# Performance work log

Measured on AMD Instinct MI355X. Metric: run time of the kernel, lower is better.

The kernel has to match this reference:

```python
import jax, jax.numpy as jnp
import numpy as np

N = 100000      # number of vertices
E = 3200000     # number of directed edges (avg degree 32)
EPS = 1e-8
WEIGHT = 0.01


def setup_inputs() -> dict:
    key = jax.random.key(0)
    k1, k2, k3, k4 = jax.random.split(key, 4)
    mu0 = jax.random.normal(k1, (N, 3), dtype=jnp.float32)
    # current positions = canonical + small deformation (realistic ARAP setting)
    mu = mu0 + 0.1 * jax.random.normal(k2, (N, 3), dtype=jnp.float32)
    i = jax.random.randint(k3, (E,), 0, N, dtype=jnp.int32)
    # avoid self-edges (rest length 0 would give w = 1/eps = 1e8 and swamp the loss)
    off = jax.random.randint(k4, (E,), 1, N, dtype=jnp.int32)
    j = (i + off) % N
    edge_idx = jnp.stack([i, j], axis=0)  # (2, E)
    return {"mu0": mu0, "mu": mu, "edge_idx": edge_idx}


def reference(mu0, mu, edge_idx):
    i, j = edge_idx[0], edge_idx[1]
    rest = mu0[j] - mu0[i]        # (E,3) canonical edge vectors
    deform = mu[j] - mu[i]        # (E,3) deformed edge vectors
    w = 1.0 / (jnp.linalg.norm(rest, axis=-1) + EPS)  # (E,)
    # per-edge weighted outer product deform \otimes rest
    outer = jnp.einsum('e,ei,ej->eij', w, deform, rest)  # (E,3,3)
    # scatter-add into per-node covariance matrices
    S = jnp.zeros((mu0.shape[0], 3, 3), dtype=mu0.dtype).at[i].add(outer)  # (N,3,3)
    U, _, Vh = jnp.linalg.svd(S, full_matrices=False)
    R = U @ Vh
    det_mask = (jnp.linalg.det(R) < 0)[:, None, None]
    diag_fix = jnp.array([-1.0, 1.0, 1.0], dtype=mu0.dtype).reshape(1, 1, 3)
    Vh = jnp.where(det_mask, Vh * diag_fix, Vh)
    R = U @ Vh                      # (N,3,3) best-fit rotations
    Ri = R[i]                       # (E,3,3)
    pred = jnp.einsum('eij,ej->ei', Ri, rest)
    err = deform - pred
    loss = jnp.sum(w * jnp.sum(err * err, axis=-1)) / jnp.sum(w)
    return WEIGHT * loss
```

## Files before the change

kernel.cpp:

```cpp
#include <hip/hip_runtime.h>
#include <hip/hip_fp16.h>
#include <math.h>

#define EPS     1e-8f
#define MP      131
#define JBITS   17
#define JMASK   ((1u << JBITS) - 1u)
#define CAP     6144
#define PMAX    1024
#define ACC_T   576
#define MAXPT   11
#define BIN_T   512
#define CHUNK   8192
#define EPT     16

struct alignas(16) Pk { __half2 a, b, c; unsigned pad; };

__global__ __launch_bounds__(256) void k_prep(
    const float* __restrict__ mu0, const float* __restrict__ mu,
    Pk* __restrict__ pk, int* __restrict__ gcursor, int N, int P)
{
    int n = blockIdx.x * blockDim.x + threadIdx.x;
    if (n < P) gcursor[n] = n * CAP;
    if (n >= N) return;
    float x0 = mu0[3*n+0], y0 = mu0[3*n+1], z0 = mu0[3*n+2];
    float x1 = mu [3*n+0], y1 = mu [3*n+1], z1 = mu [3*n+2];
    Pk o;
    o.a = __floats2half2_rn(x0, y0);
    o.b = __floats2half2_rn(z0, x1);
    o.c = __floats2half2_rn(y1, z1);
    o.pad = 0u;
    pk[n] = o;
}

__global__ __launch_bounds__(BIN_T) void k_bin(
    const int* __restrict__ ei, const int* __restrict__ ej,
    int* __restrict__ gcursor, unsigned* __restrict__ bucket,
    int E, int P)
{
    __shared__ int cnt[PMAX];
    __shared__ int dbase[PMAX];
    __shared__ int scan_tmp[PMAX];
    __shared__ int wtot[8];
    __shared__ unsigned sortw[CHUNK];
    __shared__ unsigned short sortp[CHUNK];

    int lo = blockIdx.x * CHUNK;
    int hi = lo + CHUNK; if (hi > E) hi = E;
    int ce = hi - lo;
    int tid = threadIdx.x;

    for (int t = tid; t < PMAX; t += BIN_T) cnt[t] = 0;

    int myi[EPT], myj[EPT];
    #pragma unroll
    for (int k = 0; k < EPT; ++k) {
        int e = lo + tid + k * BIN_T;
        if (e < hi) {
            myi[k] = __builtin_nontemporal_load(&ei[e]);
            myj[k] = __builtin_nontemporal_load(&ej[e]);
        } else myi[k] = -1;
    }
    __syncthreads();

    #pragma unroll
    for (int k = 0; k < EPT; ++k)
        if (myi[k] >= 0) atomicAdd(&cnt[(unsigned)myi[k] / (unsigned)MP], 1);
    __syncthreads();

    {
        int b0 = 2 * tid;
        int v1 = cnt[b0 + 1];
        int s  = cnt[b0] + v1;
        int incl = s;
        #pragma unroll
        for (int d = 1; d < 64; d <<= 1) {
            int o = __shfl_up(incl, d);
            if ((tid & 63) >= d) incl += o;
        }
        int w = tid >> 6;
        if ((tid & 63) == 63) wtot[w] = incl;
        __syncthreads();
        int base = 0;
        #pragma unroll
        for (int k = 0; k < 8; ++k) base += (k < w) ? wtot[k] : 0;
        scan_tmp[b0]     = base + incl - v1;
        scan_tmp[b0 + 1] = base + incl;
        __syncthreads();
    }

    for (int t = tid; t < P; t += BIN_T) {
        int c = cnt[t];
        int excl = scan_tmp[t] - c;
        int b = c ? atomicAdd(&gcursor[t], c) : 0;
        dbase[t] = b - excl;
        cnt[t] = excl;
    }
    __syncthreads();

    #pragma unroll
    for (int k = 0; k < EPT; ++k) {
        if (myi[k] >= 0) {
            int i = myi[k];
            int p = (int)((unsigned)i / (unsigned)MP);
            int li = i - p * MP;
            int pos = atomicAdd(&cnt[p], 1);
            sortw[pos] = ((unsigned)li << JBITS) | (unsigned)myj[k];
            sortp[pos] = (unsigned short)p;
        }
    }
    __syncthreads();

    for (int s = tid; s < ce; s += BIN_T) {
        unsigned w = sortw[s];
        int p = sortp[s];
        int dst = dbase[p] + s;
        if (dst < (p + 1) * CAP)
            bucket[dst] = w;
    }
}

__global__ __launch_bounds__(ACC_T) void k_accum(
    const Pk* __restrict__ pk,
    const unsigned* __restrict__ bucket, const int* __restrict__ gcursor,
    double* __restrict__ pblk, int N)
{
    __shared__ unsigned sorted[CAP];
    __shared__ int hist[MP];
    __shared__ int offs[MP];
    __shared__ int cursor[MP];
    __shared__ int sc[192];
    __shared__ float Sl[MP * 9];
    __shared__ double redw[9], rede[9];

    int p = blockIdx.x;
    int lo_n = p * MP;
    int beg = p * CAP;
    int end = gcursor[p];
    int cap_end = beg + CAP;
    if (end > cap_end) end = cap_end;

    for (int t = threadIdx.x; t < MP; t += ACC_T) hist[t] = 0;
    __syncthreads();

    unsigned myu[MAXPT];
    int mycnt = 0;
    {
        int e = beg + threadIdx.x;
        #pragma unroll
        for (int k = 0; k < MAXPT; ++k) {
            if (e < end) {
                unsigned uu = bucket[e];
                myu[k] = uu;
                atomicAdd(&hist[uu >> JBITS], 1);
                ++mycnt;
            }
            e += ACC_T;
        }
    }
    __syncthreads();

    if (threadIdx.x < 192) {
        int v = (threadIdx.x < MP) ? hist[threadIdx.x] : 0;
        int incl = v;
        #pragma unroll
        for (int d = 1; d < 64; d <<= 1) {
            int o = __shfl_up(incl, d);
            if ((threadIdx.x & 63) >= d) incl += o;
        }
        sc[threadIdx.x] = incl;
    }
    __syncthreads();
    if (threadIdx.x < MP) {
        int w = threadIdx.x >> 6;
        int carry = 0;
        if (w >= 1) carry += sc[63];
        if (w >= 2) carry += sc[127];
        int excl = sc[threadIdx.x] - hist[threadIdx.x] + carry;
        offs[threadIdx.x] = excl;
        cursor[threadIdx.x] = excl;
    }
    __syncthreads();

    #pragma unroll
    for (int k = 0; k < MAXPT; ++k) {
        if (k < mycnt) {
            unsigned uu = myu[k];
            int li = (int)(uu >> JBITS);
            int pos = atomicAdd(&cursor[li], 1);
            sorted[pos] = uu;
        }
    }
    __syncthreads();

    double wsum = 0.0, errsum = 0.0;
    float S[9] = {0.f,0.f,0.f,0.f,0.f,0.f,0.f,0.f,0.f};
    {
        int node = threadIdx.x >> 2;
        int part = threadIdx.x & 3;
        int n = lo_n + node;
        if (node < MP && n < N) {
            Pk ac = pk[n];
            float2 a01 = __half22float2(ac.a);
            float2 a23 = __half22float2(ac.b);
            float2 a45 = __half22float2(ac.c);
            float ax = a01.x, ay = a01.y, az = a23.x;
            float cx = a23.y, cy = a45.x, cz = a45.y;

            auto body = [&](const Pk& cc) {
                float2 f01 = __half22float2(cc.a);
                float2 f23 = __half22float2(cc.b);
                float2 f45 = __half22float2(cc.c);
                float r0 = f01.x - ax, r1 = f01.y - ay, r2 = f23.x - az;
                float d0 = f23.y - cx, d1 = f45.x - cy, d2 = f45.y - cz;
                float rr = r0*r0 + r1*r1 + r2*r2;
                float dd = d0*d0 + d1*d1 + d2*d2;
                float w  = 1.0f / (sqrtf(rr) + EPS);
                wsum   += (double)w;
                errsum += (double)(w * (dd + rr));
                float wd0 = w*d0, wd1 = w*d1, wd2 = w*d2;
                S[0] += wd0*r0; S[1] += wd0*r1; S[2] += wd0*r2;
                S[3] += wd1*r0; S[4] += wd1*r1; S[5] += wd1*r2;
                S[6] += wd2*r0; S[7] += wd2*r1; S[8] += wd2*r2;
            };

            int b0 = offs[node];
            int e1 = b0 + hist[node];
            int e  = b0 + part;
            for (; e + 12 < e1; e += 16) {
                unsigned u0 = sorted[e];
                unsigned u1 = sorted[e + 4];
                unsigned u2 = sorted[e + 8];
                unsigned u3 = sorted[e + 12];
                Pk c0 = pk[u0 & JMASK];
                Pk c1 = pk[u1 & JMASK];
                Pk c2 = pk[u2 & JMASK];
                Pk c3 = pk[u3 & JMASK];
                body(c0); body(c1); body(c2); body(c3);
            }
            for (; e + 4 < e1; e += 8) {
                unsigned u0 = sorted[e], u1 = sorted[e + 4];
                Pk c0 = pk[u0 & JMASK];
                Pk c1 = pk[u1 & JMASK];
                body(c0);
                body(c1);
            }
            if (e < e1) {
                Pk c0 = pk[sorted[e] & JMASK];
                body(c0);
            }
        }
        #pragma unroll
        for (int c = 0; c < 9; ++c) {
            S[c] += __shfl_down(S[c], 2);
            S[c] += __shfl_down(S[c], 1);
        }
        if (part == 0 && node < MP)
            #pragma unroll
            for (int c = 0; c < 9; ++c) Sl[node*9 + c] = S[c];
    }
    __syncthreads();

    if (threadIdx.x < MP && lo_n + (int)threadIdx.x < N) {
        float Sf[9], X[9];
        #pragma unroll
        for (int c = 0; c < 9; ++c) { Sf[c] = Sl[threadIdx.x*9 + c]; X[c] = Sf[c]; }
        bool ok = true;
        #pragma unroll
        for (int it = 0; it < 8; ++it) {
            float c00 =  (X[4]*X[8] - X[5]*X[7]);
            float c01 = -(X[3]*X[8] - X[5]*X[6]);
            float c02 =  (X[3]*X[7] - X[4]*X[6]);
            float c10 = -(X[1]*X[8] - X[2]*X[7]);
            float c11 =  (X[0]*X[8] - X[2]*X[6]);
            float c12 = -(X[0]*X[7] - X[1]*X[6]);
            float c20 =  (X[1]*X[5] - X[2]*X[4]);
            float c21 = -(X[0]*X[5] - X[2]*X[3]);
            float c22 =  (X[0]*X[4] - X[1]*X[3]);
            float det = X[0]*c00 + X[1]*c01 + X[2]*c02;
            if (!(fabsf(det) > 1e-30f)) { ok = false; break; }
            float inv_det = 1.0f / det;
            float Y[9] = { c00*inv_det, c01*inv_det, c02*inv_det,
                           c10*inv_det, c11*inv_det, c12*inv_det,
                           c20*inv_det, c21*inv_det, c22*inv_det };
            float nx = 0.f, ny = 0.f;
            #pragma unroll
            for (int c = 0; c < 9; ++c) { nx += X[c]*X[c]; ny += Y[c]*Y[c]; }
            float g = sqrtf(sqrtf(ny / nx));
            float hg = 0.5f * g, hig = 0.5f / g;
            #pragma unroll
            for (int c = 0; c < 9; ++c) X[c] = hg * X[c] + hig * Y[c];
        }
        if (!ok) {
            X[0]=1.f; X[1]=0.f; X[2]=0.f;
            X[3]=0.f; X[4]=1.f; X[5]=0.f;
            X[6]=0.f; X[7]=0.f; X[8]=1.f;
        }
        float det = X[0]*(X[4]*X[8] - X[5]*X[7])
                  - X[1]*(X[3]*X[8] - X[5]*X[6])
                  + X[2]*(X[3]*X[7] - X[4]*X[6]);
        if (det < 0.f) { X[0] = -X[0]; X[3] = -X[3]; X[6] = -X[6]; }
        float tr = X[0]*Sf[0] + X[1]*Sf[1] + X[2]*Sf[2]
                 + X[3]*Sf[3] + X[4]*Sf[4] + X[5]*Sf[5]
                 + X[6]*Sf[6] + X[7]*Sf[7] + X[8]*Sf[8];
        errsum -= 2.0 * (double)tr;
    }

    #pragma unroll
    for (int off = 32; off > 0; off >>= 1) {
        wsum   += __shfl_down(wsum, off);
        errsum += __shfl_down(errsum, off);
    }
    if ((threadIdx.x & 63) == 0) {
        redw[threadIdx.x >> 6] = wsum;
        rede[threadIdx.x >> 6] = errsum;
    }
    __syncthreads();
    if (threadIdx.x == 0) {
        double W = 0.0, Er = 0.0;
        #pragma unroll
        for (int k = 0; k < 9; ++k) { W += redw[k]; Er += rede[k]; }
        pblk[2*p]   = W;
        pblk[2*p+1] = Er;
    }
}

__global__ __launch_bounds__(256) void k_final(
    const double* __restrict__ pblk, int nb, float* __restrict__ out)
{
    __shared__ double sw[4], se[4];
    double w = 0.0, e = 0.0;
    for (int t = threadIdx.x; t < nb; t += 256) {
        w += pblk[2*t];
        e += pblk[2*t+1];
    }
    #pragma unroll
    for (int off = 32; off > 0; off >>= 1) {
        w += __shfl_down(w, off);
        e += __shfl_down(e, off);
    }
    if ((threadIdx.x & 63) == 0) {
        sw[threadIdx.x >> 6] = w;
        se[threadIdx.x >> 6] = e;
    }
    __syncthreads();
    if (threadIdx.x == 0) {
        double W  = sw[0] + sw[1] + sw[2] + sw[3];
        double Er = se[0] + se[1] + se[2] + se[3];
        out[0] = (float)(0.01 * (Er / W));
    }
}

extern "C" void kernel_launch(void* const* d_in, const int* in_sizes, int n_in,
                              void* d_out, int out_size, void* d_ws, size_t ws_size,
                              hipStream_t stream) {
    const float* mu0 = (const float*)d_in[0];
    const float* mu  = (const float*)d_in[1];
    const int*   eidx = (const int*)d_in[2];
    int N = in_sizes[0] / 3;
    int E = in_sizes[2] / 2;
    const int* ei = eidx;
    const int* ej = eidx + E;

    int P = (N + MP - 1) / MP;

    double*   pblk    = (double*)d_ws;
    int*      gcursor = (int*)((char*)d_ws + 2 * PMAX * sizeof(double));
    Pk*       pk      = (Pk*)((char*)d_ws + 2 * PMAX * sizeof(double) + PMAX * sizeof(int));
    unsigned* bucket  = (unsigned*)(pk + N);

    int nbin = (E + CHUNK - 1) / CHUNK;

    k_prep  <<<(N + 255) / 256, 256, 0, stream>>>(mu0, mu, pk, gcursor, N, P);
    k_bin   <<<nbin, BIN_T, 0, stream>>>(ei, ej, gcursor, bucket, E, P);
    k_accum <<<P, ACC_T, 0, stream>>>(pk, bucket, gcursor, pblk, N);
    k_final <<<1, 256, 0, stream>>>(pblk, P, (float*)d_out);
}
```

Measured before the change: 139.7 us.

## Replace block-local binning with per-edge global atomics on padded cursors

The binning kernel no longer counts, scans and sorts edges in shared memory before a coalesced write. Each thread now takes one edge and claims a slot with a global atomicAdd on its partition cursor, and the cursors are padded to one per 64 bytes to avoid false sharing. The accumulate loop is also unrolled from 4 to 8 outstanding gathers. This removes the shared-memory scan and sort and their syncs, at the cost of about 3.2M global atomics on 764 hot addresses and scattered bucket writes.

```diff
diff --git a/kernel.cpp b/kernel.cpp
--- a/kernel.cpp
+++ b/kernel.cpp
@@ -8,11 +8,9 @@
 #define JMASK   ((1u << JBITS) - 1u)
 #define CAP     6144
 #define PMAX    1024
+#define GCS     16
 #define ACC_T   576
 #define MAXPT   11
-#define BIN_T   512
-#define CHUNK   8192
-#define EPT     16
 
 struct alignas(16) Pk { __half2 a, b, c; unsigned pad; };
 
@@ -21,7 +19,7 @@
     Pk* __restrict__ pk, int* __restrict__ gcursor, int N, int P)
 {
     int n = blockIdx.x * blockDim.x + threadIdx.x;
-    if (n < P) gcursor[n] = n * CAP;
+    if (n < P) gcursor[n * GCS] = n * CAP;
     if (n >= N) return;
     float x0 = mu0[3*n+0], y0 = mu0[3*n+1], z0 = mu0[3*n+2];
     float x1 = mu [3*n+0], y1 = mu [3*n+1], z1 = mu [3*n+2];
@@ -33,91 +31,19 @@
     pk[n] = o;
 }
 
-__global__ __launch_bounds__(BIN_T) void k_bin(
+__global__ __launch_bounds__(256) void k_bin(
     const int* __restrict__ ei, const int* __restrict__ ej,
-    int* __restrict__ gcursor, unsigned* __restrict__ bucket,
-    int E, int P)
+    int* __restrict__ gcursor, unsigned* __restrict__ bucket, int E)
 {
-    __shared__ int cnt[PMAX];
-    __shared__ int dbase[PMAX];
-    __shared__ int scan_tmp[PMAX];
-    __shared__ int wtot[8];
-    __shared__ unsigned sortw[CHUNK];
-    __shared__ unsigned short sortp[CHUNK];
-
-    int lo = blockIdx.x * CHUNK;
-    int hi = lo + CHUNK; if (hi > E) hi = E;
-    int ce = hi - lo;
-    int tid = threadIdx.x;
-
-    for (int t = tid; t < PMAX; t += BIN_T) cnt[t] = 0;
-
-    int myi[EPT], myj[EPT];
-    #pragma unroll
-    for (int k = 0; k < EPT; ++k) {
-        int e = lo + tid + k * BIN_T;
-        if (e < hi) {
-            myi[k] = __builtin_nontemporal_load(&ei[e]);
-            myj[k] = __builtin_nontemporal_load(&ej[e]);
-        } else myi[k] = -1;
-    }
-    __syncthreads();
-
-    #pragma unroll
-    for (int k = 0; k < EPT; ++k)
-        if (myi[k] >= 0) atomicAdd(&cnt[(unsigned)myi[k] / (unsigned)MP], 1);
-    __syncthreads();
-
-    {
-        int b0 = 2 * tid;
-        int v1 = cnt[b0 + 1];
-        int s  = cnt[b0] + v1;
-        int incl = s;
-        #pragma unroll
-        for (int d = 1; d < 64; d <<= 1) {
-            int o = __shfl_up(incl, d);
-            if ((tid & 63) >= d) incl += o;
-        }
-        int w = tid >> 6;
-        if ((tid & 63) == 63) wtot[w] = incl;
-        __syncthreads();
-        int base = 0;
-        #pragma unroll
-        for (int k = 0; k < 8; ++k) base += (k < w) ? wtot[k] : 0;
-        scan_tmp[b0]     = base + incl - v1;
-        scan_tmp[b0 + 1] = base + incl;
-        __syncthreads();
-    }
-
-    for (int t = tid; t < P; t += BIN_T) {
-        int c = cnt[t];
-        int excl = scan_tmp[t] - c;
-        int b = c ? atomicAdd(&gcursor[t], c) : 0;
-        dbase[t] = b - excl;
-        cnt[t] = excl;
-    }
-    __syncthreads();
-
-    #pragma unroll
-    for (int k = 0; k < EPT; ++k) {
-        if (myi[k] >= 0) {
-            int i = myi[k];
-            int p = (int)((unsigned)i / (unsigned)MP);
-            int li = i - p * MP;
-            int pos = atomicAdd(&cnt[p], 1);
-            sortw[pos] = ((unsigned)li << JBITS) | (unsigned)myj[k];
-            sortp[pos] = (unsigned short)p;
-        }
-    }
-    __syncthreads();
-
-    for (int s = tid; s < ce; s += BIN_T) {
-        unsigned w = sortw[s];
-        int p = sortp[s];
-        int dst = dbase[p] + s;
-        if (dst < (p + 1) * CAP)
-            bucket[dst] = w;
-    }
+    int e = blockIdx.x * 256 + threadIdx.x;
+    if (e >= E) return;
+    int i = __builtin_nontemporal_load(&ei[e]);
+    int j = __builtin_nontemporal_load(&ej[e]);
+    unsigned p = (unsigned)i / (unsigned)MP;
+    int li = i - (int)p * MP;
+    int pos = atomicAdd(&gcursor[p * GCS], 1);
+    if (pos < (int)(p + 1) * CAP)
+        bucket[pos] = ((unsigned)li << JBITS) | (unsigned)j;
 }
 
 __global__ __launch_bounds__(ACC_T) void k_accum(
@@ -136,7 +62,7 @@
     int p = blockIdx.x;
     int lo_n = p * MP;
     int beg = p * CAP;
-    int end = gcursor[p];
+    int end = gcursor[p * GCS];
     int cap_end = beg + CAP;
     if (end > cap_end) end = cap_end;
 
@@ -227,16 +153,25 @@
             int b0 = offs[node];
             int e1 = b0 + hist[node];
             int e  = b0 + part;
-            for (; e + 12 < e1; e += 16) {
+            for (; e + 28 < e1; e += 32) {
                 unsigned u0 = sorted[e];
                 unsigned u1 = sorted[e + 4];
                 unsigned u2 = sorted[e + 8];
                 unsigned u3 = sorted[e + 12];
+                unsigned u4 = sorted[e + 16];
+                unsigned u5 = sorted[e + 20];
+                unsigned u6 = sorted[e + 24];
+                unsigned u7 = sorted[e + 28];
                 Pk c0 = pk[u0 & JMASK];
                 Pk c1 = pk[u1 & JMASK];
                 Pk c2 = pk[u2 & JMASK];
                 Pk c3 = pk[u3 & JMASK];
+                Pk c4 = pk[u4 & JMASK];
+                Pk c5 = pk[u5 & JMASK];
+                Pk c6 = pk[u6 & JMASK];
+                Pk c7 = pk[u7 & JMASK];
                 body(c0); body(c1); body(c2); body(c3);
+                body(c4); body(c5); body(c6); body(c7);
             }
             for (; e + 4 < e1; e += 8) {
                 unsigned u0 = sorted[e], u1 = sorted[e + 4];
@@ -366,13 +301,12 @@
 
     double*   pblk    = (double*)d_ws;
     int*      gcursor = (int*)((char*)d_ws + 2 * PMAX * sizeof(double));
-    Pk*       pk      = (Pk*)((char*)d_ws + 2 * PMAX * sizeof(double) + PMAX * sizeof(int));
+    Pk*       pk      = (Pk*)((char*)d_ws + 2 * PMAX * sizeof(double)
+                                          + PMAX * GCS * sizeof(int));
     unsigned* bucket  = (unsigned*)(pk + N);
 
-    int nbin = (E + CHUNK - 1) / CHUNK;
-
     k_prep  <<<(N + 255) / 256, 256, 0, stream>>>(mu0, mu, pk, gcursor, N, P);
-    k_bin   <<<nbin, BIN_T, 0, stream>>>(ei, ej, gcursor, bucket, E, P);
+    k_bin   <<<(E + 255) / 256, 256, 0, stream>>>(ei, ej, gcursor, bucket, E);
     k_accum <<<P, ACC_T, 0, stream>>>(pk, bucket, gcursor, pblk, N);
     k_final <<<1, 256, 0, stream>>>(pblk, P, (float*)d_out);
 }
```

Result: slower. 291.9 us (+109.0%).

## Replace atomic global bucket cursors with deterministic histogram, column-scan and scatter passes

Applied to the files above, without the earlier changes.

Binning becomes three passes. A per-chunk histogram kernel also packs the node data, a per-partition column scan computes exact global offsets, and a scatter kernel writes edges to those offsets. This removes the global atomics on bucket cursors, makes the bucket layout contiguous and deterministic, and lets the per-partition capacity and registers-per-thread shrink. It also widens the accumulation unroll to 8 gathers and keeps per-thread weight and error sums in float instead of double, at the cost of an extra launch, a second read of the source index array, and some precision.

```diff
diff --git a/kernel.cpp b/kernel.cpp
--- a/kernel.cpp
+++ b/kernel.cpp
@@ -6,73 +6,122 @@
 #define MP      131
 #define JBITS   17
 #define JMASK   ((1u << JBITS) - 1u)
-#define CAP     6144
+#define CAP     5120
 #define PMAX    1024
+#define OTS     768
+#define NBMAX   512
 #define ACC_T   576
-#define MAXPT   11
+#define MAXPT   9
 #define BIN_T   512
 #define CHUNK   8192
 #define EPT     16
 
 struct alignas(16) Pk { __half2 a, b, c; unsigned pad; };
 
-__global__ __launch_bounds__(256) void k_prep(
+__global__ __launch_bounds__(BIN_T) void k_hist(
     const float* __restrict__ mu0, const float* __restrict__ mu,
-    Pk* __restrict__ pk, int* __restrict__ gcursor, int N, int P)
+    Pk* __restrict__ pk, const int* __restrict__ ei,
+    int* __restrict__ cntT, int E, int N, int P)
 {
-    int n = blockIdx.x * blockDim.x + threadIdx.x;
-    if (n < P) gcursor[n] = n * CAP;
-    if (n >= N) return;
-    float x0 = mu0[3*n+0], y0 = mu0[3*n+1], z0 = mu0[3*n+2];
-    float x1 = mu [3*n+0], y1 = mu [3*n+1], z1 = mu [3*n+2];
-    Pk o;
-    o.a = __floats2half2_rn(x0, y0);
-    o.b = __floats2half2_rn(z0, x1);
-    o.c = __floats2half2_rn(y1, z1);
-    o.pad = 0u;
-    pk[n] = o;
-}
-
-__global__ __launch_bounds__(BIN_T) void k_bin(
+    __shared__ int cnt[PMAX];
+    int tid = threadIdx.x;
+
+    for (int n = blockIdx.x * BIN_T + tid; n < N; n += gridDim.x * BIN_T) {
+        float x0 = mu0[3*n+0], y0 = mu0[3*n+1], z0 = mu0[3*n+2];
+        float x1 = mu [3*n+0], y1 = mu [3*n+1], z1 = mu [3*n+2];
+        Pk o;
+        o.a = __floats2half2_rn(x0, y0);
+        o.b = __floats2half2_rn(z0, x1);
+        o.c = __floats2half2_rn(y1, z1);
+        o.pad = 0u;
+        pk[n] = o;
+    }
+
+    for (int t = tid; t < PMAX; t += BIN_T) cnt[t] = 0;
+    __syncthreads();
+
+    int lo = blockIdx.x * CHUNK;
+    int hi = lo + CHUNK; if (hi > E) hi = E;
+    #pragma unroll
+    for (int k = 0; k < EPT; ++k) {
+        int e = lo + tid + k * BIN_T;
+        if (e < hi) {
+            int i = __builtin_nontemporal_load(&ei[e]);
+            atomicAdd(&cnt[(unsigned)i / (unsigned)MP], 1);
+        }
+    }
+    __syncthreads();
+
+    size_t bo = (size_t)blockIdx.x * OTS;
+    for (int t = tid; t < P; t += BIN_T) cntT[bo + t] = cnt[t];
+}
+
+__global__ __launch_bounds__(BIN_T) void k_colscan(
+    const int* __restrict__ cntT, int* __restrict__ gofs,
+    int* __restrict__ tend, int nbin)
+{
+    __shared__ int wtot[8];
+    int p = blockIdx.x;
+    int t = threadIdx.x;
+    int v = (t < nbin) ? cntT[(size_t)t * OTS + p] : 0;
+    int incl = v;
+    #pragma unroll
+    for (int d = 1; d < 64; d <<= 1) {
+        int o = __shfl_up(incl, d);
+        if ((t & 63) >= d) incl += o;
+    }
+    int w = t >> 6;
+    if ((t & 63) == 63) wtot[w] = incl;
+    __syncthreads();
+    int base = 0;
+    #pragma unroll
+    for (int k = 0; k < 8; ++k) base += (k < w) ? wtot[k] : 0;
+    int excl = base + incl - v;
+    if (t < nbin) gofs[(size_t)t * OTS + p] = p * CAP + excl;
+    if (t == nbin - 1) tend[p] = p * CAP + excl + v;
+}
+
+__global__ __launch_bounds__(BIN_T) void k_scatter(
     const int* __restrict__ ei, const int* __restrict__ ej,
-    int* __restrict__ gcursor, unsigned* __restrict__ bucket,
+    const int* __restrict__ gofs, unsigned* __restrict__ bucket,
     int E, int P)
 {
     __shared__ int cnt[PMAX];
     __shared__ int dbase[PMAX];
-    __shared__ int scan_tmp[PMAX];
     __shared__ int wtot[8];
     __shared__ unsigned sortw[CHUNK];
     __shared__ unsigned short sortp[CHUNK];
 
+    int tid = threadIdx.x;
     int lo = blockIdx.x * CHUNK;
     int hi = lo + CHUNK; if (hi > E) hi = E;
     int ce = hi - lo;
-    int tid = threadIdx.x;
 
     for (int t = tid; t < PMAX; t += BIN_T) cnt[t] = 0;
 
-    int myi[EPT], myj[EPT];
+    int myp[EPT]; unsigned myw[EPT];
     #pragma unroll
     for (int k = 0; k < EPT; ++k) {
         int e = lo + tid + k * BIN_T;
         if (e < hi) {
-            myi[k] = __builtin_nontemporal_load(&ei[e]);
-            myj[k] = __builtin_nontemporal_load(&ej[e]);
-        } else myi[k] = -1;
+            int i = __builtin_nontemporal_load(&ei[e]);
+            int j = __builtin_nontemporal_load(&ej[e]);
+            unsigned p = (unsigned)i / (unsigned)MP;
+            myp[k] = (int)p;
+            myw[k] = (((unsigned)i - p * MP) << JBITS) | (unsigned)j;
+        } else myp[k] = -1;
     }
     __syncthreads();
 
     #pragma unroll
     for (int k = 0; k < EPT; ++k)
-        if (myi[k] >= 0) atomicAdd(&cnt[(unsigned)myi[k] / (unsigned)MP], 1);
+        if (myp[k] >= 0) atomicAdd(&cnt[myp[k]], 1);
     __syncthreads();
 
     {
-        int b0 = 2 * tid;
-        int v1 = cnt[b0 + 1];
-        int s  = cnt[b0] + v1;
-        int incl = s;
+        int b0 = 2 * tid, b1 = b0 + 1;
+        int v0 = cnt[b0], v1 = cnt[b1];
+        int incl = v0 + v1;
         #pragma unroll
         for (int d = 1; d < 64; d <<= 1) {
             int o = __shfl_up(incl, d);
@@ -84,45 +133,42 @@
         int base = 0;
         #pragma unroll
         for (int k = 0; k < 8; ++k) base += (k < w) ? wtot[k] : 0;
-        scan_tmp[b0]     = base + incl - v1;
-        scan_tmp[b0 + 1] = base + incl;
-        __syncthreads();
-    }
-
-    for (int t = tid; t < P; t += BIN_T) {
-        int c = cnt[t];
-        int excl = scan_tmp[t] - c;
-        int b = c ? atomicAdd(&gcursor[t], c) : 0;
-        dbase[t] = b - excl;
-        cnt[t] = excl;
+        int inc1 = base + incl;
+        int inc0 = inc1 - v1;
+        cnt[b0] = inc0 - v0;
+        cnt[b1] = inc1 - v1;
+    }
+    __syncthreads();
+
+    {
+        size_t bo = (size_t)blockIdx.x * OTS;
+        for (int t = tid; t < P; t += BIN_T)
+            dbase[t] = gofs[bo + t] - cnt[t];
     }
     __syncthreads();
 
     #pragma unroll
     for (int k = 0; k < EPT; ++k) {
-        if (myi[k] >= 0) {
-            int i = myi[k];
-            int p = (int)((unsigned)i / (unsigned)MP);
-            int li = i - p * MP;
-            int pos = atomicAdd(&cnt[p], 1);
-            sortw[pos] = ((unsigned)li << JBITS) | (unsigned)myj[k];
-            sortp[pos] = (unsigned short)p;
+        if (myp[k] >= 0) {
+            int pos = atomicAdd(&cnt[myp[k]], 1);
+            sortw[pos] = myw[k];
+            sortp[pos] = (unsigned short)myp[k];
         }
     }
     __syncthreads();
 
     for (int s = tid; s < ce; s += BIN_T) {
-        unsigned w = sortw[s];
+        unsigned wv = sortw[s];
         int p = sortp[s];
         int dst = dbase[p] + s;
         if (dst < (p + 1) * CAP)
-            bucket[dst] = w;
+            bucket[dst] = wv;
     }
 }
 
 __global__ __launch_bounds__(ACC_T) void k_accum(
     const Pk* __restrict__ pk,
-    const unsigned* __restrict__ bucket, const int* __restrict__ gcursor,
+    const unsigned* __restrict__ bucket, const int* __restrict__ tend,
     double* __restrict__ pblk, int N)
 {
     __shared__ unsigned sorted[CAP];
@@ -136,7 +182,7 @@
     int p = blockIdx.x;
     int lo_n = p * MP;
     int beg = p * CAP;
-    int end = gcursor[p];
+    int end = tend[p];
     int cap_end = beg + CAP;
     if (end > cap_end) end = cap_end;
 
@@ -188,7 +234,7 @@
             unsigned uu = myu[k];
             int li = (int)(uu >> JBITS);
             int pos = atomicAdd(&cursor[li], 1);
-            sorted[pos] = uu;
+            if (pos < CAP) sorted[pos] = uu;
         }
     }
     __syncthreads();
@@ -199,6 +245,7 @@
         int node = threadIdx.x >> 2;
         int part = threadIdx.x & 3;
         int n = lo_n + node;
+        float ws = 0.f, es = 0.f;
         if (node < MP && n < N) {
             Pk ac = pk[n];
             float2 a01 = __half22float2(ac.a);
@@ -216,8 +263,8 @@
                 float rr = r0*r0 + r1*r1 + r2*r2;
                 float dd = d0*d0 + d1*d1 + d2*d2;
                 float w  = 1.0f / (sqrtf(rr) + EPS);
-                wsum   += (double)w;
-                errsum += (double)(w * (dd + rr));
+                ws += w;
+                es += w * (dd + rr);
                 float wd0 = w*d0, wd1 = w*d1, wd2 = w*d2;
                 S[0] += wd0*r0; S[1] += wd0*r1; S[2] += wd0*r2;
                 S[3] += wd1*r0; S[4] += wd1*r1; S[5] += wd1*r2;
@@ -226,17 +273,27 @@
 
             int b0 = offs[node];
             int e1 = b0 + hist[node];
+            if (e1 > CAP) e1 = CAP;
             int e  = b0 + part;
-            for (; e + 12 < e1; e += 16) {
+            for (; e + 28 < e1; e += 32) {
                 unsigned u0 = sorted[e];
                 unsigned u1 = sorted[e + 4];
                 unsigned u2 = sorted[e + 8];
                 unsigned u3 = sorted[e + 12];
+                unsigned u4 = sorted[e + 16];
+                unsigned u5 = sorted[e + 20];
+                unsigned u6 = sorted[e + 24];
+                unsigned u7 = sorted[e + 28];
                 Pk c0 = pk[u0 & JMASK];
                 Pk c1 = pk[u1 & JMASK];
                 Pk c2 = pk[u2 & JMASK];
                 Pk c3 = pk[u3 & JMASK];
+                Pk c4 = pk[u4 & JMASK];
+                Pk c5 = pk[u5 & JMASK];
+                Pk c6 = pk[u6 & JMASK];
+                Pk c7 = pk[u7 & JMASK];
                 body(c0); body(c1); body(c2); body(c3);
+                body(c4); body(c5); body(c6); body(c7);
             }
             for (; e + 4 < e1; e += 8) {
                 unsigned u0 = sorted[e], u1 = sorted[e + 4];
@@ -250,6 +307,8 @@
                 body(c0);
             }
         }
+        wsum = (double)ws;
+        errsum = (double)es;
         #pragma unroll
         for (int c = 0; c < 9; ++c) {
             S[c] += __shfl_down(S[c], 2);
@@ -363,16 +422,19 @@
     const int* ej = eidx + E;
 
     int P = (N + MP - 1) / MP;
-
-    double*   pblk    = (double*)d_ws;
-    int*      gcursor = (int*)((char*)d_ws + 2 * PMAX * sizeof(double));
-    Pk*       pk      = (Pk*)((char*)d_ws + 2 * PMAX * sizeof(double) + PMAX * sizeof(int));
-    unsigned* bucket  = (unsigned*)(pk + N);
-
     int nbin = (E + CHUNK - 1) / CHUNK;
 
-    k_prep  <<<(N + 255) / 256, 256, 0, stream>>>(mu0, mu, pk, gcursor, N, P);
-    k_bin   <<<nbin, BIN_T, 0, stream>>>(ei, ej, gcursor, bucket, E, P);
-    k_accum <<<P, ACC_T, 0, stream>>>(pk, bucket, gcursor, pblk, N);
-    k_final <<<1, 256, 0, stream>>>(pblk, P, (float*)d_out);
-}
+    char* wp = (char*)d_ws;
+    double* pblk = (double*)wp;                 wp += 2 * PMAX * sizeof(double);
+    int*    tend = (int*)wp;                    wp += PMAX * sizeof(int);
+    int*    cntT = (int*)wp;                    wp += (size_t)NBMAX * OTS * sizeof(int);
+    int*    gofs = (int*)wp;                    wp += (size_t)NBMAX * OTS * sizeof(int);
+    Pk*     pk   = (Pk*)wp;                     wp += (size_t)N * sizeof(Pk);
+    unsigned* bucket = (unsigned*)wp;
+
+    k_hist    <<<nbin, BIN_T, 0, stream>>>(mu0, mu, pk, ei, cntT, E, N, P);
+    k_colscan <<<P, BIN_T, 0, stream>>>(cntT, gofs, tend, nbin);
+    k_scatter <<<nbin, BIN_T, 0, stream>>>(ei, ej, gofs, bucket, E, P);
+    k_accum   <<<P, ACC_T, 0, stream>>>(pk, bucket, tend, pblk, N);
+    k_final   <<<1, 256, 0, stream>>>(pblk, P, (float*)d_out);
+}
```

Result: slower. 154.7 us (+10.7%).

## Shrink node partitions, pad global cursors, fuse final reduction into accumulate kernel

Applied to the files above, without the earlier changes.

Partition size drops from 131 to 64 nodes, so there are about twice as many accumulate blocks of 256 threads with a 64-lane scan and a smaller per-partition capacity. Global bucket cursors are spaced 16 ints apart so atomics from different partitions do not contend on the same cache line. The separate final-reduction kernel is replaced by a last-block-done reduction driven by an atomic counter. Per-edge sums now accumulate in float before the double reduction. This raises parallelism and removes one launch, at the cost of a tighter capacity bound of 2560 edges per partition and slightly lower accumulation precision.

```diff
diff --git a/kernel.cpp b/kernel.cpp
--- a/kernel.cpp
+++ b/kernel.cpp
@@ -2,26 +2,29 @@
 #include <hip/hip_fp16.h>
 #include <math.h>
 
-#define EPS     1e-8f
-#define MP      131
-#define JBITS   17
-#define JMASK   ((1u << JBITS) - 1u)
-#define CAP     6144
-#define PMAX    1024
-#define ACC_T   576
-#define MAXPT   11
-#define BIN_T   512
-#define CHUNK   8192
-#define EPT     16
+#define EPS    1e-8f
+#define MP     64
+#define JBITS  17
+#define JMASK  ((1u << JBITS) - 1u)
+#define CAP    2560
+#define PM2    2048
+#define GCS    16
+#define BIN_T  512
+#define CHUNK  8192
+#define EPT    16
+#define ACC_T  256
+#define MAXPT  10
 
 struct alignas(16) Pk { __half2 a, b, c; unsigned pad; };
 
 __global__ __launch_bounds__(256) void k_prep(
     const float* __restrict__ mu0, const float* __restrict__ mu,
-    Pk* __restrict__ pk, int* __restrict__ gcursor, int N, int P)
+    Pk* __restrict__ pk, int* __restrict__ gcursor, int* __restrict__ gb,
+    int N)
 {
     int n = blockIdx.x * blockDim.x + threadIdx.x;
-    if (n < P) gcursor[n] = n * CAP;
+    if (n == 0) gb[0] = 0;
+    for (int t = n; t < PM2 * GCS; t += gridDim.x * blockDim.x) gcursor[t] = 0;
     if (n >= N) return;
     float x0 = mu0[3*n+0], y0 = mu0[3*n+1], z0 = mu0[3*n+2];
     float x1 = mu [3*n+0], y1 = mu [3*n+1], z1 = mu [3*n+2];
@@ -38,40 +41,42 @@
     int* __restrict__ gcursor, unsigned* __restrict__ bucket,
     int E, int P)
 {
-    __shared__ int cnt[PMAX];
-    __shared__ int dbase[PMAX];
-    __shared__ int scan_tmp[PMAX];
+    __shared__ int cnt[PM2];
+    __shared__ int dbase[PM2];
     __shared__ int wtot[8];
     __shared__ unsigned sortw[CHUNK];
     __shared__ unsigned short sortp[CHUNK];
 
+    int tid = threadIdx.x;
     int lo = blockIdx.x * CHUNK;
     int hi = lo + CHUNK; if (hi > E) hi = E;
     int ce = hi - lo;
-    int tid = threadIdx.x;
-
-    for (int t = tid; t < PMAX; t += BIN_T) cnt[t] = 0;
-
-    int myi[EPT], myj[EPT];
+
+    for (int t = tid; t < PM2; t += BIN_T) cnt[t] = 0;
+
+    int myp[EPT]; unsigned myw[EPT];
     #pragma unroll
     for (int k = 0; k < EPT; ++k) {
         int e = lo + tid + k * BIN_T;
         if (e < hi) {
-            myi[k] = __builtin_nontemporal_load(&ei[e]);
-            myj[k] = __builtin_nontemporal_load(&ej[e]);
-        } else myi[k] = -1;
+            int i = __builtin_nontemporal_load(&ei[e]);
+            int j = __builtin_nontemporal_load(&ej[e]);
+            unsigned p = (unsigned)i / (unsigned)MP;
+            myp[k] = (int)p;
+            myw[k] = (((unsigned)i - p * MP) << JBITS) | (unsigned)j;
+        } else myp[k] = -1;
     }
     __syncthreads();
 
     #pragma unroll
     for (int k = 0; k < EPT; ++k)
-        if (myi[k] >= 0) atomicAdd(&cnt[(unsigned)myi[k] / (unsigned)MP], 1);
+        if (myp[k] >= 0) atomicAdd(&cnt[myp[k]], 1);
     __syncthreads();
 
     {
-        int b0 = 2 * tid;
-        int v1 = cnt[b0 + 1];
-        int s  = cnt[b0] + v1;
+        int q = 4 * tid;
+        int v0 = cnt[q], v1 = cnt[q+1], v2 = cnt[q+2], v3 = cnt[q+3];
+        int s = v0 + v1 + v2 + v3;
         int incl = s;
         #pragma unroll
         for (int d = 1; d < 64; d <<= 1) {
@@ -84,69 +89,66 @@
         int base = 0;
         #pragma unroll
         for (int k = 0; k < 8; ++k) base += (k < w) ? wtot[k] : 0;
-        scan_tmp[b0]     = base + incl - v1;
-        scan_tmp[b0 + 1] = base + incl;
-        __syncthreads();
-    }
-
-    for (int t = tid; t < P; t += BIN_T) {
-        int c = cnt[t];
-        int excl = scan_tmp[t] - c;
-        int b = c ? atomicAdd(&gcursor[t], c) : 0;
-        dbase[t] = b - excl;
-        cnt[t] = excl;
+        int e0 = base + incl - s;
+        int e1 = e0 + v0;
+        int e2 = e1 + v1;
+        int e3 = e2 + v2;
+        if (v0) { int r = atomicAdd(&gcursor[(q  ) * GCS], v0); dbase[q  ] = (q  ) * CAP + r - e0; }
+        if (v1) { int r = atomicAdd(&gcursor[(q+1) * GCS], v1); dbase[q+1] = (q+1) * CAP + r - e1; }
+        if (v2) { int r = atomicAdd(&gcursor[(q+2) * GCS], v2); dbase[q+2] = (q+2) * CAP + r - e2; }
+        if (v3) { int r = atomicAdd(&gcursor[(q+3) * GCS], v3); dbase[q+3] = (q+3) * CAP + r - e3; }
+        cnt[q] = e0; cnt[q+1] = e1; cnt[q+2] = e2; cnt[q+3] = e3;
     }
     __syncthreads();
 
     #pragma unroll
     for (int k = 0; k < EPT; ++k) {
-        if (myi[k] >= 0) {
-            int i = myi[k];
-            int p = (int)((unsigned)i / (unsigned)MP);
-            int li = i - p * MP;
-            int pos = atomicAdd(&cnt[p], 1);
-            sortw[pos] = ((unsigned)li << JBITS) | (unsigned)myj[k];
-            sortp[pos] = (unsigned short)p;
+        if (myp[k] >= 0) {
+            int pos = atomicAdd(&cnt[myp[k]], 1);
+            sortw[pos] = myw[k];
+            sortp[pos] = (unsigned short)myp[k];
         }
     }
     __syncthreads();
 
     for (int s = tid; s < ce; s += BIN_T) {
-        unsigned w = sortw[s];
-        int p = sortp[s];
-        int dst = dbase[p] + s;
-        if (dst < (p + 1) * CAP)
-            bucket[dst] = w;
+        unsigned wv = sortw[s];
+        int pp = sortp[s];
+        int dst = dbase[pp] + s;
+        if (dst < (pp + 1) * CAP)
+            bucket[dst] = wv;
     }
 }
 
-__global__ __launch_bounds__(ACC_T) void k_accum(
+__global__ __launch_bounds__(ACC_T, 8) void k_accum(
     const Pk* __restrict__ pk,
     const unsigned* __restrict__ bucket, const int* __restrict__ gcursor,
-    double* __restrict__ pblk, int N)
+    double* __restrict__ pblk, int* __restrict__ gb,
+    float* __restrict__ out, int N, int P)
 {
     __shared__ unsigned sorted[CAP];
     __shared__ int hist[MP];
     __shared__ int offs[MP];
     __shared__ int cursor[MP];
-    __shared__ int sc[192];
     __shared__ float Sl[MP * 9];
-    __shared__ double redw[9], rede[9];
+    __shared__ double redw[4], rede[4];
+    __shared__ int lastf;
 
     int p = blockIdx.x;
     int lo_n = p * MP;
     int beg = p * CAP;
-    int end = gcursor[p];
-    int cap_end = beg + CAP;
-    if (end > cap_end) end = cap_end;
-
-    for (int t = threadIdx.x; t < MP; t += ACC_T) hist[t] = 0;
+    int tid = threadIdx.x;
+    int cntp = gcursor[p * GCS];
+    if (cntp > CAP) cntp = CAP;
+    int end = beg + cntp;
+
+    for (int t = tid; t < MP; t += ACC_T) hist[t] = 0;
     __syncthreads();
 
     unsigned myu[MAXPT];
     int mycnt = 0;
     {
-        int e = beg + threadIdx.x;
+        int e = beg + tid;
         #pragma unroll
         for (int k = 0; k < MAXPT; ++k) {
             if (e < end) {
@@ -160,25 +162,17 @@
     }
     __syncthreads();
 
-    if (threadIdx.x < 192) {
-        int v = (threadIdx.x < MP) ? hist[threadIdx.x] : 0;
+    if (tid < MP) {
+        int v = hist[tid];
         int incl = v;
         #pragma unroll
         for (int d = 1; d < 64; d <<= 1) {
             int o = __shfl_up(incl, d);
-            if ((threadIdx.x & 63) >= d) incl += o;
-        }
-        sc[threadIdx.x] = incl;
-    }
-    __syncthreads();
-    if (threadIdx.x < MP) {
-        int w = threadIdx.x >> 6;
-        int carry = 0;
-        if (w >= 1) carry += sc[63];
-        if (w >= 2) carry += sc[127];
-        int excl = sc[threadIdx.x] - hist[threadIdx.x] + carry;
-        offs[threadIdx.x] = excl;
-        cursor[threadIdx.x] = excl;
+            if (tid >= d) incl += o;
+        }
+        int excl = incl - v;
+        offs[tid] = excl;
+        cursor[tid] = excl;
     }
     __syncthreads();
 
@@ -186,9 +180,8 @@
     for (int k = 0; k < MAXPT; ++k) {
         if (k < mycnt) {
             unsigned uu = myu[k];
-            int li = (int)(uu >> JBITS);
-            int pos = atomicAdd(&cursor[li], 1);
-            sorted[pos] = uu;
+            int pos = atomicAdd(&cursor[uu >> JBITS], 1);
+            if (pos < CAP) sorted[pos] = uu;
         }
     }
     __syncthreads();
@@ -196,10 +189,11 @@
     double wsum = 0.0, errsum = 0.0;
     float S[9] = {0.f,0.f,0.f,0.f,0.f,0.f,0.f,0.f,0.f};
     {
-        int node = threadIdx.x >> 2;
-        int part = threadIdx.x & 3;
+        int node = tid >> 2;
+        int part = tid & 3;
         int n = lo_n + node;
-        if (node < MP && n < N) {
+        float ws = 0.f, es = 0.f;
+        if (n < N) {
             Pk ac = pk[n];
             float2 a01 = __half22float2(ac.a);
             float2 a23 = __half22float2(ac.b);
@@ -216,8 +210,8 @@
                 float rr = r0*r0 + r1*r1 + r2*r2;
                 float dd = d0*d0 + d1*d1 + d2*d2;
                 float w  = 1.0f / (sqrtf(rr) + EPS);
-                wsum   += (double)w;
-                errsum += (double)(w * (dd + rr));
+                ws += w;
+                es += w * (dd + rr);
                 float wd0 = w*d0, wd1 = w*d1, wd2 = w*d2;
                 S[0] += wd0*r0; S[1] += wd0*r1; S[2] += wd0*r2;
                 S[3] += wd1*r0; S[4] += wd1*r1; S[5] += wd1*r2;
@@ -226,6 +220,7 @@
 
             int b0 = offs[node];
             int e1 = b0 + hist[node];
+            if (e1 > CAP) e1 = CAP;
             int e  = b0 + part;
             for (; e + 12 < e1; e += 16) {
                 unsigned u0 = sorted[e];
@@ -250,21 +245,23 @@
                 body(c0);
             }
         }
+        wsum = (double)ws;
+        errsum = (double)es;
         #pragma unroll
         for (int c = 0; c < 9; ++c) {
             S[c] += __shfl_down(S[c], 2);
             S[c] += __shfl_down(S[c], 1);
         }
-        if (part == 0 && node < MP)
+        if (part == 0)
             #pragma unroll
             for (int c = 0; c < 9; ++c) Sl[node*9 + c] = S[c];
     }
     __syncthreads();
 
-    if (threadIdx.x < MP && lo_n + (int)threadIdx.x < N) {
+    if (tid < MP && lo_n + tid < N) {
         float Sf[9], X[9];
         #pragma unroll
-        for (int c = 0; c < 9; ++c) { Sf[c] = Sl[threadIdx.x*9 + c]; X[c] = Sf[c]; }
+        for (int c = 0; c < 9; ++c) { Sf[c] = Sl[tid*9 + c]; X[c] = Sf[c]; }
         bool ok = true;
         #pragma unroll
         for (int it = 0; it < 8; ++it) {
@@ -311,42 +308,41 @@
         wsum   += __shfl_down(wsum, off);
         errsum += __shfl_down(errsum, off);
     }
-    if ((threadIdx.x & 63) == 0) {
-        redw[threadIdx.x >> 6] = wsum;
-        rede[threadIdx.x >> 6] = errsum;
-    }
-    __syncthreads();
-    if (threadIdx.x == 0) {
-        double W = 0.0, Er = 0.0;
-        #pragma unroll
-        for (int k = 0; k < 9; ++k) { W += redw[k]; Er += rede[k]; }
-        pblk[2*p]   = W;
-        pblk[2*p+1] = Er;
-    }
-}
-
-__global__ __launch_bounds__(256) void k_final(
-    const double* __restrict__ pblk, int nb, float* __restrict__ out)
-{
-    __shared__ double sw[4], se[4];
-    double w = 0.0, e = 0.0;
-    for (int t = threadIdx.x; t < nb; t += 256) {
-        w += pblk[2*t];
-        e += pblk[2*t+1];
+    if ((tid & 63) == 0) {
+        redw[tid >> 6] = wsum;
+        rede[tid >> 6] = errsum;
+    }
+    __syncthreads();
+
+    if (tid == 0) {
+        double W  = redw[0] + redw[1] + redw[2] + redw[3];
+        double Er = rede[0] + rede[1] + rede[2] + rede[3];
+        __hip_atomic_store(&pblk[2*p],   W,  __ATOMIC_RELAXED, __HIP_MEMORY_SCOPE_AGENT);
+        __hip_atomic_store(&pblk[2*p+1], Er, __ATOMIC_RELAXED, __HIP_MEMORY_SCOPE_AGENT);
+        int t = __hip_atomic_fetch_add(gb, 1, __ATOMIC_ACQ_REL, __HIP_MEMORY_SCOPE_AGENT);
+        lastf = (t == P - 1) ? 1 : 0;
+    }
+    __syncthreads();
+    if (!lastf) return;
+
+    double w2 = 0.0, e2 = 0.0;
+    for (int t = tid; t < P; t += ACC_T) {
+        w2 += __hip_atomic_load(&pblk[2*t],   __ATOMIC_RELAXED, __HIP_MEMORY_SCOPE_AGENT);
+        e2 += __hip_atomic_load(&pblk[2*t+1], __ATOMIC_RELAXED, __HIP_MEMORY_SCOPE_AGENT);
     }
     #pragma unroll
     for (int off = 32; off > 0; off >>= 1) {
-        w += __shfl_down(w, off);
-        e += __shfl_down(e, off);
-    }
-    if ((threadIdx.x & 63) == 0) {
-        sw[threadIdx.x >> 6] = w;
-        se[threadIdx.x >> 6] = e;
-    }
-    __syncthreads();
-    if (threadIdx.x == 0) {
-        double W  = sw[0] + sw[1] + sw[2] + sw[3];
-        double Er = se[0] + se[1] + se[2] + se[3];
+        w2 += __shfl_down(w2, off);
+        e2 += __shfl_down(e2, off);
+    }
+    if ((tid & 63) == 0) {
+        redw[tid >> 6] = w2;
+        rede[tid >> 6] = e2;
+    }
+    __syncthreads();
+    if (tid == 0) {
+        double W  = redw[0] + redw[1] + redw[2] + redw[3];
+        double Er = rede[0] + rede[1] + rede[2] + rede[3];
         out[0] = (float)(0.01 * (Er / W));
     }
 }
@@ -362,17 +358,18 @@
     const int* ei = eidx;
     const int* ej = eidx + E;
 
-    int P = (N + MP - 1) / MP;
-
-    double*   pblk    = (double*)d_ws;
-    int*      gcursor = (int*)((char*)d_ws + 2 * PMAX * sizeof(double));
-    Pk*       pk      = (Pk*)((char*)d_ws + 2 * PMAX * sizeof(double) + PMAX * sizeof(int));
-    unsigned* bucket  = (unsigned*)(pk + N);
-
+    int P    = (N + MP - 1) / MP;
     int nbin = (E + CHUNK - 1) / CHUNK;
 
-    k_prep  <<<(N + 255) / 256, 256, 0, stream>>>(mu0, mu, pk, gcursor, N, P);
+    char* wp = (char*)d_ws;
+    int*      gb      = (int*)wp;        wp += 256;
+    double*   pblk    = (double*)wp;     wp += (size_t)2 * PM2 * sizeof(double);
+    int*      gcursor = (int*)wp;        wp += (size_t)PM2 * GCS * sizeof(int);
+    Pk*       pk      = (Pk*)wp;         wp += (size_t)N * sizeof(Pk);
+    unsigned* bucket  = (unsigned*)wp;
+
+    k_prep  <<<(N + 255) / 256, 256, 0, stream>>>(mu0, mu, pk, gcursor, gb, N);
     k_bin   <<<nbin, BIN_T, 0, stream>>>(ei, ej, gcursor, bucket, E, P);
-    k_accum <<<P, ACC_T, 0, stream>>>(pk, bucket, gcursor, pblk, N);
-    k_final <<<1, 256, 0, stream>>>(pblk, P, (float*)d_out);
+    k_accum <<<P, ACC_T, 0, stream>>>(pk, bucket, gcursor, pblk, gb,
+                                      (float*)d_out, N, P);
 }
```

Result: slower. 209.1 us (+49.7%).
